# Kernel optimization log

Measured on AMD Instinct MI355X. Metric: run time of the kernel, lower is better.

The kernel has to match this reference:

```python
import jax, jax.numpy as jnp
import numpy as np

B, H, S, D = 2, 16, 2048, 64
NUM_BUCKETS = 32
MAX_DISTANCE = 256


def setup_inputs() -> dict:
    key = jax.random.key(0)
    kq, kk, kv, kb, kl = jax.random.split(key, 5)
    q = jax.random.normal(kq, (B, H, S, D), dtype=jnp.float32)
    k = jax.random.normal(kk, (B, H, S, D), dtype=jnp.float32)
    v = jax.random.normal(kv, (B, H, S, D), dtype=jnp.float32)
    bias_table = jax.random.normal(kb, (NUM_BUCKETS, H), dtype=jnp.float32)
    event_length = jax.random.randint(kl, (B,), 1, S + 1, dtype=jnp.int64)
    return {"q": q, "k": k, "v": v, "bias_table": bias_table, "event_length": event_length}


def _relative_position_bucket(relative_position):
    # T5-style bucketing exactly as the torch module: n = -rel_pos
    half = NUM_BUCKETS // 2  # 16
    n = -relative_position
    is_small = n < half
    # guard log for the branch not taken (n<=0); where() masks it out
    nf = jnp.maximum(n, 1).astype(jnp.float32)
    val_if_large = half + jnp.minimum(
        jnp.log(nf / half) / np.log(MAX_DISTANCE / half) * (NUM_BUCKETS - half),
        NUM_BUCKETS - 1 - half,
    ).astype(jnp.int32)
    ret = jnp.where(is_small, n, val_if_large)
    return jnp.clip(ret, 0, NUM_BUCKETS - 1)


def _compute_bias(bias_table, seq_len):
    ctx = jnp.arange(seq_len)[:, None]
    mem = jnp.arange(seq_len)[None, :]
    rp_bucket = _relative_position_bucket(mem - ctx)  # (S,S)
    values = bias_table[rp_bucket]                    # (S,S,H)
    return jnp.transpose(values, (2, 0, 1))[None]     # (1,H,S,S)


def reference(q, k, v, bias_table, event_length):
    seq_len = q.shape[2]
    head_dim = q.shape[3]
    # scaled QK^T: (B,H,S,S)
    logits = jnp.einsum("bhsd,bhtd->bhst", q, k) / np.sqrt(head_dim).astype(np.float32)
    logits = logits + _compute_bias(bias_table, seq_len)
    # key-side padding mask from per-event lengths
    mask = jnp.arange(seq_len)[None, None, None, :] < event_length[:, None, None, None]
    logits = jnp.where(mask, logits, jnp.float32(-1e9))
    attn = jax.nn.softmax(logits, axis=-1)
    # dropout p=0.01 omitted (eval-mode deterministic reference)
    return jnp.einsum("bhst,bhtd->bhsd", attn, v)
```

## Files before the change

kernel.cpp:

```cpp
#include <hip/hip_runtime.h>

#define B_ 2
#define H_ 16
#define S_ 2048
#define D_ 64
#define BQ 128
#define BK 64
#define NQB (S_ / BQ)
#define LDSTR 72
#define LOG2E 1.4426950408889634f
#define FIXM 10.0f

#if __has_builtin(__builtin_amdgcn_exp2f)
#define EXP2F(x) __builtin_amdgcn_exp2f(x)
#else
#define EXP2F(x) __expf((x) * 0.6931471805599453f)
#endif

typedef _Float16 half8 __attribute__((ext_vector_type(8)));
typedef _Float16 half4 __attribute__((ext_vector_type(4)));
typedef __fp16   fp16x2 __attribute__((ext_vector_type(2)));
typedef float floatx4 __attribute__((ext_vector_type(4)));

typedef _Float16 KlArr[BK][LDSTR];
typedef _Float16 VtArr[D_][LDSTR];
typedef _Float16 PlArr[32][LDSTR];

#define VT_OFF  18432
#define PL_OFF  36864
#define LUT_OFF 55296
#define OX_STR  66
#define LX_OFF  33792

__global__ __launch_bounds__(512, 4)
void t5_attn_kernel(const float* __restrict__ qg_, const float* __restrict__ kg_,
                    const float* __restrict__ vg_, const float* __restrict__ bt,
                    const int* __restrict__ elen, float* __restrict__ outg_)
{
    __shared__ __align__(16) unsigned char smem[56320];
    KlArr* Kl  = reinterpret_cast<KlArr*>(smem);
    VtArr* Vt  = reinterpret_cast<VtArr*>(smem + VT_OFF);
    PlArr* Pl  = reinterpret_cast<PlArr*>(smem + PL_OFF);
    float* lut = reinterpret_cast<float*>(smem + LUT_OFF);

    const int tid  = threadIdx.x;
    const int wave = tid >> 6;
    const int lane = tid & 63;
    const int quad = lane >> 4;
    const int t16  = lane & 15;
    const int wq   = wave >> 1;
    const int kh   = wave & 1;

    const int f    = blockIdx.x + NQB * (blockIdx.y + H_ * blockIdx.z);
    const int qblk = (f >> 3) & 15;
    const int bh   = (f & 7) | ((f >> 7) << 3);
    const int h    = bh & 15;
    const int b    = bh >> 4;

    if (tid < 256) {
        int n = tid;
        int bucket;
        if (n < 16) {
            bucket = n;
        } else {
            int vl = (int)(__log2f((float)n * 0.0625f) * 4.0f);
            bucket = 16 + (vl < 15 ? vl : 15);
        }
        lut[n] = bt[bucket * H_ + h] * LOG2E - FIXM;
    }
    const float sh_next = FIXM - bt[h] * LOG2E;
    const float sh_far  = FIXM - bt[31 * H_ + h] * LOG2E;

    const int len = (elen[1] == 0) ? elen[2 * b] : elen[b];
    const int ntiles = (len + BK - 1) >> 6;

    const size_t bhoff = ((size_t)b * H_ + h) * (size_t)(S_ * D_);
    const float* qptr = qg_ + bhoff;
    const float* kptr = kg_ + bhoff;
    const float* vptr = vg_ + bhoff;
    float*       optr = outg_ + bhoff;

    half8 qf[2][2];
    {
        const float qscale = 0.125f * LOG2E;
        #pragma unroll
        for (int rg = 0; rg < 2; ++rg) {
            const int row = qblk * BQ + wq * 32 + rg * 16 + t16;
            const float* qp = qptr + (size_t)row * D_ + quad * 8;
            #pragma unroll
            for (int c = 0; c < 2; ++c) {
                const float4* p = reinterpret_cast<const float4*>(qp + c * 32);
                float4 x0 = p[0], x1 = p[1];
                half8 hv;
                hv[0] = (_Float16)(x0.x * qscale); hv[1] = (_Float16)(x0.y * qscale);
                hv[2] = (_Float16)(x0.z * qscale); hv[3] = (_Float16)(x0.w * qscale);
                hv[4] = (_Float16)(x1.x * qscale); hv[5] = (_Float16)(x1.y * qscale);
                hv[6] = (_Float16)(x1.z * qscale); hv[7] = (_Float16)(x1.w * qscale);
                qf[rg][c] = hv;
            }
        }
    }

    floatx4 zero4 = {0.f, 0.f, 0.f, 0.f};
    floatx4 acc[2][4];
    float l_[2];
    #pragma unroll
    for (int rg = 0; rg < 2; ++rg) {
        #pragma unroll
        for (int nb = 0; nb < 4; ++nb) acc[rg][nb] = zero4;
        l_[rg] = 0.f;
    }

    const int i_lo = qblk * BQ + wq * 32;

    float4 kx[2];
    float  vx[8];
    auto prefetch = [&](int kt) {
        const int row = tid >> 3;
        const int c8  = (tid & 7) << 3;
        const float4* p = reinterpret_cast<const float4*>(
            kptr + ((size_t)(kt * BK + row) * D_ + c8));
        kx[0] = p[0];
        kx[1] = p[1];
        const int key8 = kt * BK + wave * 8;
        #pragma unroll
        for (int jj = 0; jj < 8; ++jj)
            vx[jj] = vptr[(size_t)(key8 + jj) * D_ + lane];
    };
    auto stage = [&](int buf) {
        const int row = tid >> 3;
        const int c8  = (tid & 7) << 3;
        half8 hv;
        hv[0]=(_Float16)kx[0].x; hv[1]=(_Float16)kx[0].y; hv[2]=(_Float16)kx[0].z; hv[3]=(_Float16)kx[0].w;
        hv[4]=(_Float16)kx[1].x; hv[5]=(_Float16)kx[1].y; hv[6]=(_Float16)kx[1].z; hv[7]=(_Float16)kx[1].w;
        *reinterpret_cast<half8*>(&Kl[buf][row][c8]) = hv;
        half8 vv;
        #pragma unroll
        for (int jj = 0; jj < 8; ++jj) vv[jj] = (_Float16)vx[jj];
        *reinterpret_cast<half8*>(&Vt[buf][lane][wave * 8]) = vv;
    };

    prefetch(0);
    stage(0);
    __syncthreads();

    for (int kt = 0; kt < ntiles; ++kt) {
        const int cur = kt & 1;
        const bool more = (kt + 1) < ntiles;
        if (more) prefetch(kt + 1);

        const int keybase = kt * BK + kh * 32;

        floatx4 sa[2][2];
        #pragma unroll
        for (int rg = 0; rg < 2; ++rg)
            #pragma unroll
            for (int nb = 0; nb < 2; ++nb) sa[rg][nb] = zero4;
        #pragma unroll
        for (int kc = 0; kc < 2; ++kc) {
            #pragma unroll
            for (int nb = 0; nb < 2; ++nb) {
                half8 af = *reinterpret_cast<const half8*>(
                    &Kl[cur][kh * 32 + nb * 16 + t16][kc * 32 + quad * 8]);
                sa[0][nb] = __builtin_amdgcn_mfma_f32_16x16x32_f16(af, qf[0][kc], sa[0][nb], 0, 0, 0);
                sa[1][nb] = __builtin_amdgcn_mfma_f32_16x16x32_f16(af, qf[1][kc], sa[1][nb], 0, 0, 0);
            }
        }

        if (i_lo + 31 <= keybase) {
            #pragma unroll
            for (int rg = 0; rg < 2; ++rg)
                #pragma unroll
                for (int nb = 0; nb < 2; ++nb)
                    #pragma unroll
                    for (int r = 0; r < 4; ++r) sa[rg][nb][r] -= sh_next;
        } else if (i_lo >= keybase + 247) {
            #pragma unroll
            for (int rg = 0; rg < 2; ++rg)
                #pragma unroll
                for (int nb = 0; nb < 2; ++nb)
                    #pragma unroll
                    for (int r = 0; r < 4; ++r) sa[rg][nb][r] -= sh_far;
        } else {
            #pragma unroll
            for (int rg = 0; rg < 2; ++rg) {
                const int d0 = i_lo + rg * 16 + t16 - keybase - quad * 4;
                #pragma unroll
                for (int nb = 0; nb < 2; ++nb) {
                    #pragma unroll
                    for (int r = 0; r < 4; ++r) {
                        int d = d0 - nb * 16 - r;
                        d = d < 0 ? 0 : (d > 255 ? 255 : d);
                        sa[rg][nb][r] += lut[d];
                    }
                }
            }
        }
        if ((kt == ntiles - 1) && (len & 63)) {
            #pragma unroll
            for (int nb = 0; nb < 2; ++nb) {
                #pragma unroll
                for (int r = 0; r < 4; ++r) {
                    bool valid = (keybase + nb * 16 + quad * 4 + r) < len;
                    #pragma unroll
                    for (int rg = 0; rg < 2; ++rg)
                        sa[rg][nb][r] = valid ? sa[rg][nb][r] : -1e30f;
                }
            }
        }

        #pragma unroll
        for (int rg = 0; rg < 2; ++rg) {
            float s = 0.f;
            #pragma unroll
            for (int nb = 0; nb < 2; ++nb)
                #pragma unroll
                for (int r = 0; r < 4; ++r) {
                    sa[rg][nb][r] = EXP2F(sa[rg][nb][r]);
                    s += sa[rg][nb][r];
                }
            l_[rg] += s;
        }

        #pragma unroll
        for (int rg = 0; rg < 2; ++rg) {
            #pragma unroll
            for (int nb = 0; nb < 2; ++nb) {
                fp16x2 lo = __builtin_amdgcn_cvt_pkrtz(sa[rg][nb][0], sa[rg][nb][1]);
                fp16x2 hi = __builtin_amdgcn_cvt_pkrtz(sa[rg][nb][2], sa[rg][nb][3]);
                half4 w;
                w[0] = (_Float16)lo[0]; w[1] = (_Float16)lo[1];
                w[2] = (_Float16)hi[0]; w[3] = (_Float16)hi[1];
                *reinterpret_cast<half4*>(
                    &Pl[wq][rg * 16 + t16][kh * 32 + nb * 16 + quad * 4]) = w;
            }
        }
        asm volatile("s_waitcnt lgkmcnt(0)" ::: "memory");

        {
            half8 a0 = *reinterpret_cast<const half8*>(
                &Pl[wq][t16][kh * 32 + quad * 8]);
            half8 a1 = *reinterpret_cast<const half8*>(
                &Pl[wq][16 + t16][kh * 32 + quad * 8]);
            #pragma unroll
            for (int nb = 0; nb < 4; ++nb) {
                half8 bv = *reinterpret_cast<const half8*>(
                    &Vt[cur][nb * 16 + t16][kh * 32 + quad * 8]);
                acc[0][nb] = __builtin_amdgcn_mfma_f32_16x16x32_f16(a0, bv, acc[0][nb], 0, 0, 0);
                acc[1][nb] = __builtin_amdgcn_mfma_f32_16x16x32_f16(a1, bv, acc[1][nb], 0, 0, 0);
            }
        }

        if (more) stage(cur ^ 1);
        __syncthreads();
    }

    float lh[2];
    #pragma unroll
    for (int rg = 0; rg < 2; ++rg) {
        float lv = l_[rg];
        lv += __shfl_xor(lv, 16, 64);
        lv += __shfl_xor(lv, 32, 64);
        lh[rg] = lv;
    }
    float* Ox = reinterpret_cast<float*>(smem);
    float* Lx = reinterpret_cast<float*>(smem + LX_OFF);
    if (kh == 1) {
        #pragma unroll
        for (int rg = 0; rg < 2; ++rg) {
            #pragma unroll
            for (int nb = 0; nb < 4; ++nb)
                #pragma unroll
                for (int r = 0; r < 4; ++r)
                    Ox[(wq * 32 + rg * 16 + quad * 4 + r) * OX_STR + nb * 16 + t16] =
                        acc[rg][nb][r];
            if (quad == 0) Lx[wq * 32 + rg * 16 + t16] = lh[rg];
        }
    }
    __syncthreads();
    if (kh == 0) {
        #pragma unroll
        for (int rg = 0; rg < 2; ++rg) {
            const float inv = 1.f / (lh[rg] + Lx[wq * 32 + rg * 16 + t16]);
            #pragma unroll
            for (int r = 0; r < 4; ++r) {
                const int rowloc = quad * 4 + r;
                const float invr = __shfl(inv, (lane & 48) | rowloc, 64);
                const int row = qblk * BQ + wq * 32 + rg * 16 + rowloc;
                #pragma unroll
                for (int nb = 0; nb < 4; ++nb)
                    optr[(size_t)row * D_ + nb * 16 + t16] =
                        (acc[rg][nb][r] +
                         Ox[(wq * 32 + rg * 16 + rowloc) * OX_STR + nb * 16 + t16]) * invr;
            }
        }
    }
}

extern "C" void kernel_launch(void* const* d_in, const int* in_sizes, int n_in,
                              void* d_out, int out_size, void* d_ws, size_t ws_size,
                              hipStream_t stream) {
    const float* q  = (const float*)d_in[0];
    const float* k  = (const float*)d_in[1];
    const float* v  = (const float*)d_in[2];
    const float* bt = (const float*)d_in[3];
    const int*   el = (const int*)d_in[4];
    float* out = (float*)d_out;
    dim3 grid(NQB, H_, B_);
    t5_attn_kernel<<<grid, 512, 0, stream>>>(q, k, v, bt, el, out);
}
```

Baseline: 121.9 us.

## Halve query block to 64 rows per block and remap 1-D grid

Shrinks each block's query tile from 128 to 64 rows, so each wave handles one 16-row group instead of two. This doubles the number of blocks, lowers register and LDS use, and raises the occupancy hint to 6 blocks per CU. The grid becomes 1-D with a new bit mapping that keeps blocks sharing the same batch/head close together for L2 reuse. The cost is that every K/V tile is loaded and converted to fp16 twice as often per query row, and the MFMA work per synchronisation halves.

```diff
diff --git a/kernel.cpp b/kernel.cpp
--- a/kernel.cpp
+++ b/kernel.cpp
@@ -4,7 +4,7 @@
 #define H_ 16
 #define S_ 2048
 #define D_ 64
-#define BQ 128
+#define BQ 64
 #define BK 64
 #define NQB (S_ / BQ)
 #define LDSTR 72
@@ -24,20 +24,20 @@
 
 typedef _Float16 KlArr[BK][LDSTR];
 typedef _Float16 VtArr[D_][LDSTR];
-typedef _Float16 PlArr[32][LDSTR];
+typedef _Float16 PlArr[16][LDSTR];
 
 #define VT_OFF  18432
 #define PL_OFF  36864
-#define LUT_OFF 55296
+#define LUT_OFF 46080
 #define OX_STR  66
-#define LX_OFF  33792
-
-__global__ __launch_bounds__(512, 4)
+#define LX_OFF  16896
+
+__global__ __launch_bounds__(512, 6)
 void t5_attn_kernel(const float* __restrict__ qg_, const float* __restrict__ kg_,
                     const float* __restrict__ vg_, const float* __restrict__ bt,
                     const int* __restrict__ elen, float* __restrict__ outg_)
 {
-    __shared__ __align__(16) unsigned char smem[56320];
+    __shared__ __align__(16) unsigned char smem[47104];
     KlArr* Kl  = reinterpret_cast<KlArr*>(smem);
     VtArr* Vt  = reinterpret_cast<VtArr*>(smem + VT_OFF);
     PlArr* Pl  = reinterpret_cast<PlArr*>(smem + PL_OFF);
@@ -51,11 +51,10 @@
     const int wq   = wave >> 1;
     const int kh   = wave & 1;
 
-    const int f    = blockIdx.x + NQB * (blockIdx.y + H_ * blockIdx.z);
-    const int qblk = (f >> 3) & 15;
-    const int bh   = (f & 7) | ((f >> 7) << 3);
-    const int h    = bh & 15;
-    const int b    = bh >> 4;
+    const int f    = blockIdx.x;
+    const int b    = (f >> 3) & 1;
+    const int qblk = (f >> 4) & 31;
+    const int h    = (f & 7) | (((f >> 9) & 1) << 3);
 
     if (tid < 256) {
         int n = tid;
@@ -80,38 +79,31 @@
     const float* vptr = vg_ + bhoff;
     float*       optr = outg_ + bhoff;
 
-    half8 qf[2][2];
+    half8 qf[2];
     {
         const float qscale = 0.125f * LOG2E;
-        #pragma unroll
-        for (int rg = 0; rg < 2; ++rg) {
-            const int row = qblk * BQ + wq * 32 + rg * 16 + t16;
-            const float* qp = qptr + (size_t)row * D_ + quad * 8;
-            #pragma unroll
-            for (int c = 0; c < 2; ++c) {
-                const float4* p = reinterpret_cast<const float4*>(qp + c * 32);
-                float4 x0 = p[0], x1 = p[1];
-                half8 hv;
-                hv[0] = (_Float16)(x0.x * qscale); hv[1] = (_Float16)(x0.y * qscale);
-                hv[2] = (_Float16)(x0.z * qscale); hv[3] = (_Float16)(x0.w * qscale);
-                hv[4] = (_Float16)(x1.x * qscale); hv[5] = (_Float16)(x1.y * qscale);
-                hv[6] = (_Float16)(x1.z * qscale); hv[7] = (_Float16)(x1.w * qscale);
-                qf[rg][c] = hv;
-            }
+        const int row = qblk * BQ + wq * 16 + t16;
+        const float* qp = qptr + (size_t)row * D_ + quad * 8;
+        #pragma unroll
+        for (int c = 0; c < 2; ++c) {
+            const float4* p = reinterpret_cast<const float4*>(qp + c * 32);
+            float4 x0 = p[0], x1 = p[1];
+            half8 hv;
+            hv[0] = (_Float16)(x0.x * qscale); hv[1] = (_Float16)(x0.y * qscale);
+            hv[2] = (_Float16)(x0.z * qscale); hv[3] = (_Float16)(x0.w * qscale);
+            hv[4] = (_Float16)(x1.x * qscale); hv[5] = (_Float16)(x1.y * qscale);
+            hv[6] = (_Float16)(x1.z * qscale); hv[7] = (_Float16)(x1.w * qscale);
+            qf[c] = hv;
         }
     }
 
     floatx4 zero4 = {0.f, 0.f, 0.f, 0.f};
-    floatx4 acc[2][4];
-    float l_[2];
+    floatx4 acc[4];
+    float l_ = 0.f;
     #pragma unroll
-    for (int rg = 0; rg < 2; ++rg) {
-        #pragma unroll
-        for (int nb = 0; nb < 4; ++nb) acc[rg][nb] = zero4;
-        l_[rg] = 0.f;
-    }
-
-    const int i_lo = qblk * BQ + wq * 32;
+    for (int nb = 0; nb < 4; ++nb) acc[nb] = zero4;
+
+    const int i_lo = qblk * BQ + wq * 16;
 
     float4 kx[2];
     float  vx[8];
@@ -151,48 +143,37 @@
 
         const int keybase = kt * BK + kh * 32;
 
-        floatx4 sa[2][2];
-        #pragma unroll
-        for (int rg = 0; rg < 2; ++rg)
-            #pragma unroll
-            for (int nb = 0; nb < 2; ++nb) sa[rg][nb] = zero4;
+        floatx4 sa[2];
+        sa[0] = zero4; sa[1] = zero4;
         #pragma unroll
         for (int kc = 0; kc < 2; ++kc) {
             #pragma unroll
             for (int nb = 0; nb < 2; ++nb) {
                 half8 af = *reinterpret_cast<const half8*>(
                     &Kl[cur][kh * 32 + nb * 16 + t16][kc * 32 + quad * 8]);
-                sa[0][nb] = __builtin_amdgcn_mfma_f32_16x16x32_f16(af, qf[0][kc], sa[0][nb], 0, 0, 0);
-                sa[1][nb] = __builtin_amdgcn_mfma_f32_16x16x32_f16(af, qf[1][kc], sa[1][nb], 0, 0, 0);
-            }
-        }
-
-        if (i_lo + 31 <= keybase) {
-            #pragma unroll
-            for (int rg = 0; rg < 2; ++rg)
-                #pragma unroll
-                for (int nb = 0; nb < 2; ++nb)
-                    #pragma unroll
-                    for (int r = 0; r < 4; ++r) sa[rg][nb][r] -= sh_next;
+                sa[nb] = __builtin_amdgcn_mfma_f32_16x16x32_f16(af, qf[kc], sa[nb], 0, 0, 0);
+            }
+        }
+
+        if (i_lo + 15 <= keybase) {
+            #pragma unroll
+            for (int nb = 0; nb < 2; ++nb)
+                #pragma unroll
+                for (int r = 0; r < 4; ++r) sa[nb][r] -= sh_next;
         } else if (i_lo >= keybase + 247) {
             #pragma unroll
-            for (int rg = 0; rg < 2; ++rg)
-                #pragma unroll
-                for (int nb = 0; nb < 2; ++nb)
-                    #pragma unroll
-                    for (int r = 0; r < 4; ++r) sa[rg][nb][r] -= sh_far;
+            for (int nb = 0; nb < 2; ++nb)
+                #pragma unroll
+                for (int r = 0; r < 4; ++r) sa[nb][r] -= sh_far;
         } else {
-            #pragma unroll
-            for (int rg = 0; rg < 2; ++rg) {
-                const int d0 = i_lo + rg * 16 + t16 - keybase - quad * 4;
-                #pragma unroll
-                for (int nb = 0; nb < 2; ++nb) {
-                    #pragma unroll
-                    for (int r = 0; r < 4; ++r) {
-                        int d = d0 - nb * 16 - r;
-                        d = d < 0 ? 0 : (d > 255 ? 255 : d);
-                        sa[rg][nb][r] += lut[d];
-                    }
+            const int d0 = i_lo + t16 - keybase - quad * 4;
+            #pragma unroll
+            for (int nb = 0; nb < 2; ++nb) {
+                #pragma unroll
+                for (int r = 0; r < 4; ++r) {
+                    int d = d0 - nb * 16 - r;
+                    d = d < 0 ? 0 : (d > 255 ? 255 : d);
+                    sa[nb][r] += lut[d];
                 }
             }
         }
@@ -202,52 +183,43 @@
                 #pragma unroll
                 for (int r = 0; r < 4; ++r) {
                     bool valid = (keybase + nb * 16 + quad * 4 + r) < len;
-                    #pragma unroll
-                    for (int rg = 0; rg < 2; ++rg)
-                        sa[rg][nb][r] = valid ? sa[rg][nb][r] : -1e30f;
+                    sa[nb][r] = valid ? sa[nb][r] : -1e30f;
                 }
             }
         }
 
-        #pragma unroll
-        for (int rg = 0; rg < 2; ++rg) {
+        {
             float s = 0.f;
             #pragma unroll
             for (int nb = 0; nb < 2; ++nb)
                 #pragma unroll
                 for (int r = 0; r < 4; ++r) {
-                    sa[rg][nb][r] = EXP2F(sa[rg][nb][r]);
-                    s += sa[rg][nb][r];
+                    sa[nb][r] = EXP2F(sa[nb][r]);
+                    s += sa[nb][r];
                 }
-            l_[rg] += s;
-        }
-
-        #pragma unroll
-        for (int rg = 0; rg < 2; ++rg) {
-            #pragma unroll
-            for (int nb = 0; nb < 2; ++nb) {
-                fp16x2 lo = __builtin_amdgcn_cvt_pkrtz(sa[rg][nb][0], sa[rg][nb][1]);
-                fp16x2 hi = __builtin_amdgcn_cvt_pkrtz(sa[rg][nb][2], sa[rg][nb][3]);
-                half4 w;
-                w[0] = (_Float16)lo[0]; w[1] = (_Float16)lo[1];
-                w[2] = (_Float16)hi[0]; w[3] = (_Float16)hi[1];
-                *reinterpret_cast<half4*>(
-                    &Pl[wq][rg * 16 + t16][kh * 32 + nb * 16 + quad * 4]) = w;
-            }
+            l_ += s;
+        }
+
+        #pragma unroll
+        for (int nb = 0; nb < 2; ++nb) {
+            fp16x2 lo = __builtin_amdgcn_cvt_pkrtz(sa[nb][0], sa[nb][1]);
+            fp16x2 hi = __builtin_amdgcn_cvt_pkrtz(sa[nb][2], sa[nb][3]);
+            half4 w;
+            w[0] = (_Float16)lo[0]; w[1] = (_Float16)lo[1];
+            w[2] = (_Float16)hi[0]; w[3] = (_Float16)hi[1];
+            *reinterpret_cast<half4*>(
+                &Pl[wq][t16][kh * 32 + nb * 16 + quad * 4]) = w;
         }
         asm volatile("s_waitcnt lgkmcnt(0)" ::: "memory");
 
         {
             half8 a0 = *reinterpret_cast<const half8*>(
                 &Pl[wq][t16][kh * 32 + quad * 8]);
-            half8 a1 = *reinterpret_cast<const half8*>(
-                &Pl[wq][16 + t16][kh * 32 + quad * 8]);
             #pragma unroll
             for (int nb = 0; nb < 4; ++nb) {
                 half8 bv = *reinterpret_cast<const half8*>(
                     &Vt[cur][nb * 16 + t16][kh * 32 + quad * 8]);
-                acc[0][nb] = __builtin_amdgcn_mfma_f32_16x16x32_f16(a0, bv, acc[0][nb], 0, 0, 0);
-                acc[1][nb] = __builtin_amdgcn_mfma_f32_16x16x32_f16(a1, bv, acc[1][nb], 0, 0, 0);
+                acc[nb] = __builtin_amdgcn_mfma_f32_16x16x32_f16(a0, bv, acc[nb], 0, 0, 0);
             }
         }
 
@@ -255,44 +227,33 @@
         __syncthreads();
     }
 
-    float lh[2];
-    #pragma unroll
-    for (int rg = 0; rg < 2; ++rg) {
-        float lv = l_[rg];
-        lv += __shfl_xor(lv, 16, 64);
-        lv += __shfl_xor(lv, 32, 64);
-        lh[rg] = lv;
-    }
+    float lh = l_;
+    lh += __shfl_xor(lh, 16, 64);
+    lh += __shfl_xor(lh, 32, 64);
+
     float* Ox = reinterpret_cast<float*>(smem);
     float* Lx = reinterpret_cast<float*>(smem + LX_OFF);
     if (kh == 1) {
         #pragma unroll
-        for (int rg = 0; rg < 2; ++rg) {
-            #pragma unroll
-            for (int nb = 0; nb < 4; ++nb)
-                #pragma unroll
-                for (int r = 0; r < 4; ++r)
-                    Ox[(wq * 32 + rg * 16 + quad * 4 + r) * OX_STR + nb * 16 + t16] =
-                        acc[rg][nb][r];
-            if (quad == 0) Lx[wq * 32 + rg * 16 + t16] = lh[rg];
-        }
+        for (int nb = 0; nb < 4; ++nb)
+            #pragma unroll
+            for (int r = 0; r < 4; ++r)
+                Ox[(wq * 16 + quad * 4 + r) * OX_STR + nb * 16 + t16] = acc[nb][r];
+        if (quad == 0) Lx[wq * 16 + t16] = lh;
     }
     __syncthreads();
     if (kh == 0) {
-        #pragma unroll
-        for (int rg = 0; rg < 2; ++rg) {
-            const float inv = 1.f / (lh[rg] + Lx[wq * 32 + rg * 16 + t16]);
-            #pragma unroll
-            for (int r = 0; r < 4; ++r) {
-                const int rowloc = quad * 4 + r;
-                const float invr = __shfl(inv, (lane & 48) | rowloc, 64);
-                const int row = qblk * BQ + wq * 32 + rg * 16 + rowloc;
-                #pragma unroll
-                for (int nb = 0; nb < 4; ++nb)
-                    optr[(size_t)row * D_ + nb * 16 + t16] =
-                        (acc[rg][nb][r] +
-                         Ox[(wq * 32 + rg * 16 + rowloc) * OX_STR + nb * 16 + t16]) * invr;
-            }
+        const float inv = 1.f / (lh + Lx[wq * 16 + t16]);
+        #pragma unroll
+        for (int r = 0; r < 4; ++r) {
+            const int rowloc = quad * 4 + r;
+            const float invr = __shfl(inv, (lane & 48) | rowloc, 64);
+            const int row = qblk * BQ + wq * 16 + rowloc;
+            #pragma unroll
+            for (int nb = 0; nb < 4; ++nb)
+                optr[(size_t)row * D_ + nb * 16 + t16] =
+                    (acc[nb][r] +
+                     Ox[(wq * 16 + rowloc) * OX_STR + nb * 16 + t16]) * invr;
         }
     }
 }
@@ -306,6 +267,6 @@
     const float* bt = (const float*)d_in[3];
     const int*   el = (const int*)d_in[4];
     float* out = (float*)d_out;
-    dim3 grid(NQB, H_, B_);
+    dim3 grid(NQB * H_ * B_);
     t5_attn_kernel<<<grid, 512, 0, stream>>>(q, k, v, bt, el, out);
 }
```

Result: slower. 148.5 us (+21.9%).

## Balance key-tile work across batches with split-K blocks and workspace merge

Applied to the files above, without the earlier changes.

Adds a split kernel that counts the total valid key tiles across both batches and divides that tile range evenly between two blocks per (head, query block), so every block does about the same work no matter how the event lengths differ. When a block's range straddles the batch boundary, each half writes its partial numerator and row sums to a workspace slot, and an atomic counter picks whichever block finishes second to merge them and normalise. The change also adds s_setprio around the MFMA sections. The cost is an extra memset launch, workspace traffic and atomics; the path is used only when a large enough workspace is supplied.

```diff
diff --git a/kernel.cpp b/kernel.cpp
--- a/kernel.cpp
+++ b/kernel.cpp
@@ -32,6 +32,352 @@
 #define OX_STR  66
 #define LX_OFF  33792
 
+#define SLOT_F  8320
+#define WS_NEED (1024u + 512u * SLOT_F * 4u)
+
+__global__ __launch_bounds__(512, 4)
+void t5_attn_split(const float* __restrict__ qg_, const float* __restrict__ kg_,
+                   const float* __restrict__ vg_, const float* __restrict__ bt,
+                   const int* __restrict__ elen, float* __restrict__ outg_,
+                   float* __restrict__ ws)
+{
+    __shared__ __align__(16) unsigned char smem[56320];
+    __shared__ int s_old;
+    KlArr* Kl  = reinterpret_cast<KlArr*>(smem);
+    VtArr* Vt  = reinterpret_cast<VtArr*>(smem + VT_OFF);
+    PlArr* Pl  = reinterpret_cast<PlArr*>(smem + PL_OFF);
+    float* lut = reinterpret_cast<float*>(smem + LUT_OFF);
+
+    const int tid  = threadIdx.x;
+    const int wave = tid >> 6;
+    const int lane = tid & 63;
+    const int quad = lane >> 4;
+    const int t16  = lane & 15;
+    const int wq   = wave >> 1;
+    const int kh   = wave & 1;
+
+    const int f = blockIdx.x;
+    const int w = f >> 8;
+    const int p = f & 255;
+    const int h    = p & 15;
+    const int qblk = p >> 4;
+
+    if (tid < 256) {
+        int n = tid;
+        int bucket;
+        if (n < 16) {
+            bucket = n;
+        } else {
+            int vl = (int)(__log2f((float)n * 0.0625f) * 4.0f);
+            bucket = 16 + (vl < 15 ? vl : 15);
+        }
+        lut[n] = bt[bucket * H_ + h] * LOG2E - FIXM;
+    }
+    const float sh_next = FIXM - bt[h] * LOG2E;
+    const float sh_far  = FIXM - bt[31 * H_ + h] * LOG2E;
+
+    const int l0 = elen[0];
+    const int l1 = (elen[1] == 0) ? elen[2] : elen[1];
+    const int nt0 = (l0 + 63) >> 6;
+    const int nt1 = (l1 + 63) >> 6;
+    const int T    = nt0 + nt1;
+    const int half = (T + 1) >> 1;
+    const int sA = w ? half : 0;
+    const int eA = w ? T    : half;
+    const int shared_b = (half < nt0) ? 0 : ((half > nt0) ? 1 : -1);
+
+    unsigned* flags = reinterpret_cast<unsigned*>(ws);
+    float* part = ws + 256;
+
+    const int i_lo = qblk * BQ + wq * 32;
+
+    for (int bseg = 0; bseg < 2; ++bseg) {
+        const int lo = bseg ? nt0 : 0;
+        const int hi = bseg ? T   : nt0;
+        int s = sA > lo ? sA : lo;
+        int e = eA < hi ? eA : hi;
+        if (s >= e) continue;
+        const int ktA = s - lo, ktB = e - lo;
+        const int len = bseg ? l1 : l0;
+        const int ntb = bseg ? nt1 : nt0;
+        const bool is_partial = (bseg == shared_b);
+
+        const size_t bhoff = ((size_t)bseg * H_ + h) * (size_t)(S_ * D_);
+        const float* qptr = qg_ + bhoff;
+        const float* kptr = kg_ + bhoff;
+        const float* vptr = vg_ + bhoff;
+        float*       optr = outg_ + bhoff;
+
+        half8 qf[2][2];
+        {
+            const float qscale = 0.125f * LOG2E;
+            #pragma unroll
+            for (int rg = 0; rg < 2; ++rg) {
+                const int row = qblk * BQ + wq * 32 + rg * 16 + t16;
+                const float* qp = qptr + (size_t)row * D_ + quad * 8;
+                #pragma unroll
+                for (int c = 0; c < 2; ++c) {
+                    const float4* pq = reinterpret_cast<const float4*>(qp + c * 32);
+                    float4 x0 = pq[0], x1 = pq[1];
+                    half8 hv;
+                    hv[0] = (_Float16)(x0.x * qscale); hv[1] = (_Float16)(x0.y * qscale);
+                    hv[2] = (_Float16)(x0.z * qscale); hv[3] = (_Float16)(x0.w * qscale);
+                    hv[4] = (_Float16)(x1.x * qscale); hv[5] = (_Float16)(x1.y * qscale);
+                    hv[6] = (_Float16)(x1.z * qscale); hv[7] = (_Float16)(x1.w * qscale);
+                    qf[rg][c] = hv;
+                }
+            }
+        }
+
+        floatx4 zero4 = {0.f, 0.f, 0.f, 0.f};
+        floatx4 acc[2][4];
+        float l_[2];
+        #pragma unroll
+        for (int rg = 0; rg < 2; ++rg) {
+            #pragma unroll
+            for (int nb = 0; nb < 4; ++nb) acc[rg][nb] = zero4;
+            l_[rg] = 0.f;
+        }
+
+        float4 kx[2];
+        float  vx[8];
+        auto prefetch = [&](int kt) {
+            const int row = tid >> 3;
+            const int c8  = (tid & 7) << 3;
+            const float4* pp = reinterpret_cast<const float4*>(
+                kptr + ((size_t)(kt * BK + row) * D_ + c8));
+            kx[0] = pp[0];
+            kx[1] = pp[1];
+            const int key8 = kt * BK + wave * 8;
+            #pragma unroll
+            for (int jj = 0; jj < 8; ++jj)
+                vx[jj] = vptr[(size_t)(key8 + jj) * D_ + lane];
+        };
+        auto stage = [&](int buf) {
+            const int row = tid >> 3;
+            const int c8  = (tid & 7) << 3;
+            half8 hv;
+            hv[0]=(_Float16)kx[0].x; hv[1]=(_Float16)kx[0].y; hv[2]=(_Float16)kx[0].z; hv[3]=(_Float16)kx[0].w;
+            hv[4]=(_Float16)kx[1].x; hv[5]=(_Float16)kx[1].y; hv[6]=(_Float16)kx[1].z; hv[7]=(_Float16)kx[1].w;
+            *reinterpret_cast<half8*>(&Kl[buf][row][c8]) = hv;
+            half8 vv;
+            #pragma unroll
+            for (int jj = 0; jj < 8; ++jj) vv[jj] = (_Float16)vx[jj];
+            *reinterpret_cast<half8*>(&Vt[buf][lane][wave * 8]) = vv;
+        };
+
+        prefetch(ktA);
+        stage(ktA & 1);
+        __syncthreads();
+
+        for (int kt = ktA; kt < ktB; ++kt) {
+            const int cur = kt & 1;
+            const bool more = (kt + 1) < ktB;
+            if (more) prefetch(kt + 1);
+
+            const int keybase = kt * BK + kh * 32;
+
+            floatx4 sa[2][2];
+            #pragma unroll
+            for (int rg = 0; rg < 2; ++rg)
+                #pragma unroll
+                for (int nb = 0; nb < 2; ++nb) sa[rg][nb] = zero4;
+            __builtin_amdgcn_s_setprio(1);
+            #pragma unroll
+            for (int kc = 0; kc < 2; ++kc) {
+                #pragma unroll
+                for (int nb = 0; nb < 2; ++nb) {
+                    half8 af = *reinterpret_cast<const half8*>(
+                        &Kl[cur][kh * 32 + nb * 16 + t16][kc * 32 + quad * 8]);
+                    sa[0][nb] = __builtin_amdgcn_mfma_f32_16x16x32_f16(af, qf[0][kc], sa[0][nb], 0, 0, 0);
+                    sa[1][nb] = __builtin_amdgcn_mfma_f32_16x16x32_f16(af, qf[1][kc], sa[1][nb], 0, 0, 0);
+                }
+            }
+            __builtin_amdgcn_s_setprio(0);
+
+            if (i_lo + 31 <= keybase) {
+                #pragma unroll
+                for (int rg = 0; rg < 2; ++rg)
+                    #pragma unroll
+                    for (int nb = 0; nb < 2; ++nb)
+                        #pragma unroll
+                        for (int r = 0; r < 4; ++r) sa[rg][nb][r] -= sh_next;
+            } else if (i_lo >= keybase + 247) {
+                #pragma unroll
+                for (int rg = 0; rg < 2; ++rg)
+                    #pragma unroll
+                    for (int nb = 0; nb < 2; ++nb)
+                        #pragma unroll
+                        for (int r = 0; r < 4; ++r) sa[rg][nb][r] -= sh_far;
+            } else {
+                #pragma unroll
+                for (int rg = 0; rg < 2; ++rg) {
+                    const int d0 = i_lo + rg * 16 + t16 - keybase - quad * 4;
+                    #pragma unroll
+                    for (int nb = 0; nb < 2; ++nb) {
+                        #pragma unroll
+                        for (int r = 0; r < 4; ++r) {
+                            int d = d0 - nb * 16 - r;
+                            d = d < 0 ? 0 : (d > 255 ? 255 : d);
+                            sa[rg][nb][r] += lut[d];
+                        }
+                    }
+                }
+            }
+            if ((kt == ntb - 1) && (len & 63)) {
+                #pragma unroll
+                for (int nb = 0; nb < 2; ++nb) {
+                    #pragma unroll
+                    for (int r = 0; r < 4; ++r) {
+                        bool valid = (keybase + nb * 16 + quad * 4 + r) < len;
+                        #pragma unroll
+                        for (int rg = 0; rg < 2; ++rg)
+                            sa[rg][nb][r] = valid ? sa[rg][nb][r] : -1e30f;
+                    }
+                }
+            }
+
+            #pragma unroll
+            for (int rg = 0; rg < 2; ++rg) {
+                float ssum = 0.f;
+                #pragma unroll
+                for (int nb = 0; nb < 2; ++nb)
+                    #pragma unroll
+                    for (int r = 0; r < 4; ++r) {
+                        sa[rg][nb][r] = EXP2F(sa[rg][nb][r]);
+                        ssum += sa[rg][nb][r];
+                    }
+                l_[rg] += ssum;
+            }
+
+            #pragma unroll
+            for (int rg = 0; rg < 2; ++rg) {
+                #pragma unroll
+                for (int nb = 0; nb < 2; ++nb) {
+                    fp16x2 plo = __builtin_amdgcn_cvt_pkrtz(sa[rg][nb][0], sa[rg][nb][1]);
+                    fp16x2 phi = __builtin_amdgcn_cvt_pkrtz(sa[rg][nb][2], sa[rg][nb][3]);
+                    half4 wv;
+                    wv[0] = (_Float16)plo[0]; wv[1] = (_Float16)plo[1];
+                    wv[2] = (_Float16)phi[0]; wv[3] = (_Float16)phi[1];
+                    *reinterpret_cast<half4*>(
+                        &Pl[wq][rg * 16 + t16][kh * 32 + nb * 16 + quad * 4]) = wv;
+                }
+            }
+            asm volatile("s_waitcnt lgkmcnt(0)" ::: "memory");
+
+            {
+                half8 a0 = *reinterpret_cast<const half8*>(
+                    &Pl[wq][t16][kh * 32 + quad * 8]);
+                half8 a1 = *reinterpret_cast<const half8*>(
+                    &Pl[wq][16 + t16][kh * 32 + quad * 8]);
+                __builtin_amdgcn_s_setprio(1);
+                #pragma unroll
+                for (int nb = 0; nb < 4; ++nb) {
+                    half8 bv = *reinterpret_cast<const half8*>(
+                        &Vt[cur][nb * 16 + t16][kh * 32 + quad * 8]);
+                    acc[0][nb] = __builtin_amdgcn_mfma_f32_16x16x32_f16(a0, bv, acc[0][nb], 0, 0, 0);
+                    acc[1][nb] = __builtin_amdgcn_mfma_f32_16x16x32_f16(a1, bv, acc[1][nb], 0, 0, 0);
+                }
+                __builtin_amdgcn_s_setprio(0);
+            }
+
+            if (more) stage(cur ^ 1);
+            __syncthreads();
+        }
+
+        float lh[2];
+        #pragma unroll
+        for (int rg = 0; rg < 2; ++rg) {
+            float lv = l_[rg];
+            lv += __shfl_xor(lv, 16, 64);
+            lv += __shfl_xor(lv, 32, 64);
+            lh[rg] = lv;
+        }
+        float* Ox = reinterpret_cast<float*>(smem);
+        float* Lx = reinterpret_cast<float*>(smem + LX_OFF);
+        if (kh == 1) {
+            #pragma unroll
+            for (int rg = 0; rg < 2; ++rg) {
+                #pragma unroll
+                for (int nb = 0; nb < 4; ++nb)
+                    #pragma unroll
+                    for (int r = 0; r < 4; ++r)
+                        Ox[(wq * 32 + rg * 16 + quad * 4 + r) * OX_STR + nb * 16 + t16] =
+                            acc[rg][nb][r];
+                if (quad == 0) Lx[wq * 32 + rg * 16 + t16] = lh[rg];
+            }
+        }
+        __syncthreads();
+
+        if (!is_partial) {
+            if (kh == 0) {
+                #pragma unroll
+                for (int rg = 0; rg < 2; ++rg) {
+                    const float inv = 1.f / (lh[rg] + Lx[wq * 32 + rg * 16 + t16]);
+                    #pragma unroll
+                    for (int r = 0; r < 4; ++r) {
+                        const int rowloc = quad * 4 + r;
+                        const float invr = __shfl(inv, (lane & 48) | rowloc, 64);
+                        const int row = qblk * BQ + wq * 32 + rg * 16 + rowloc;
+                        #pragma unroll
+                        for (int nb = 0; nb < 4; ++nb)
+                            optr[(size_t)row * D_ + nb * 16 + t16] =
+                                (acc[rg][nb][r] +
+                                 Ox[(wq * 32 + rg * 16 + rowloc) * OX_STR + nb * 16 + t16]) * inv
+                                * 0.f + (acc[rg][nb][r] +
+                                 Ox[(wq * 32 + rg * 16 + rowloc) * OX_STR + nb * 16 + t16]) * invr;
+                    }
+                }
+            }
+        } else {
+            float* slot = part + (size_t)(p * 2 + w) * SLOT_F;
+            if (kh == 0) {
+                #pragma unroll
+                for (int rg = 0; rg < 2; ++rg) {
+                    #pragma unroll
+                    for (int r = 0; r < 4; ++r) {
+                        const int rowloc = quad * 4 + r;
+                        const int rloc = wq * 32 + rg * 16 + rowloc;
+                        #pragma unroll
+                        for (int nb = 0; nb < 4; ++nb)
+                            slot[rloc * D_ + nb * 16 + t16] =
+                                acc[rg][nb][r] +
+                                Ox[rloc * OX_STR + nb * 16 + t16];
+                    }
+                    if (quad == 0)
+                        slot[8192 + wq * 32 + rg * 16 + t16] =
+                            lh[rg] + Lx[wq * 32 + rg * 16 + t16];
+                }
+            }
+            __syncthreads();
+            if (tid == 0) {
+                __threadfence();
+                s_old = (int)atomicAdd(&flags[p], 1u);
+            }
+            __syncthreads();
+            if (s_old == 1) {
+                __threadfence();
+                const float* s0 = part + (size_t)(p * 2 + 0) * SLOT_F;
+                const float* s1 = part + (size_t)(p * 2 + 1) * SLOT_F;
+                const int row = tid >> 2;
+                const int c16 = (tid & 3) << 4;
+                const float inv = 1.f / (s0[8192 + row] + s1[8192 + row]);
+                float* od = optr + (size_t)(qblk * BQ + row) * D_ + c16;
+                #pragma unroll
+                for (int j = 0; j < 4; ++j) {
+                    float4 a = *reinterpret_cast<const float4*>(s0 + row * D_ + c16 + j * 4);
+                    float4 bvv = *reinterpret_cast<const float4*>(s1 + row * D_ + c16 + j * 4);
+                    float4 o;
+                    o.x = (a.x + bvv.x) * inv; o.y = (a.y + bvv.y) * inv;
+                    o.z = (a.z + bvv.z) * inv; o.w = (a.w + bvv.w) * inv;
+                    *reinterpret_cast<float4*>(od + j * 4) = o;
+                }
+            }
+        }
+        __syncthreads();
+    }
+}
+
 __global__ __launch_bounds__(512, 4)
 void t5_attn_kernel(const float* __restrict__ qg_, const float* __restrict__ kg_,
                     const float* __restrict__ vg_, const float* __restrict__ bt,
@@ -60,9 +406,8 @@
     if (tid < 256) {
         int n = tid;
         int bucket;
-        if (n < 16) {
-            bucket = n;
-        } else {
+        if (n < 16) bucket = n;
+        else {
             int vl = (int)(__log2f((float)n * 0.0625f) * 4.0f);
             bucket = 16 + (vl < 15 ? vl : 15);
         }
@@ -89,8 +434,8 @@
             const float* qp = qptr + (size_t)row * D_ + quad * 8;
             #pragma unroll
             for (int c = 0; c < 2; ++c) {
-                const float4* p = reinterpret_cast<const float4*>(qp + c * 32);
-                float4 x0 = p[0], x1 = p[1];
+                const float4* pq = reinterpret_cast<const float4*>(qp + c * 32);
+                float4 x0 = pq[0], x1 = pq[1];
                 half8 hv;
                 hv[0] = (_Float16)(x0.x * qscale); hv[1] = (_Float16)(x0.y * qscale);
                 hv[2] = (_Float16)(x0.z * qscale); hv[3] = (_Float16)(x0.w * qscale);
@@ -118,10 +463,10 @@
     auto prefetch = [&](int kt) {
         const int row = tid >> 3;
         const int c8  = (tid & 7) << 3;
-        const float4* p = reinterpret_cast<const float4*>(
+        const float4* pp = reinterpret_cast<const float4*>(
             kptr + ((size_t)(kt * BK + row) * D_ + c8));
-        kx[0] = p[0];
-        kx[1] = p[1];
+        kx[0] = pp[0];
+        kx[1] = pp[1];
         const int key8 = kt * BK + wave * 8;
         #pragma unroll
         for (int jj = 0; jj < 8; ++jj)
@@ -211,28 +556,28 @@
 
         #pragma unroll
         for (int rg = 0; rg < 2; ++rg) {
-            float s = 0.f;
+            float ssum = 0.f;
             #pragma unroll
             for (int nb = 0; nb < 2; ++nb)
                 #pragma unroll
                 for (int r = 0; r < 4; ++r) {
                     sa[rg][nb][r] = EXP2F(sa[rg][nb][r]);
-                    s += sa[rg][nb][r];
-                }
-            l_[rg] += s;
+                    ssum += sa[rg][nb][r];
+                }
+            l_[rg] += ssum;
         }
 
         #pragma unroll
         for (int rg = 0; rg < 2; ++rg) {
             #pragma unroll
             for (int nb = 0; nb < 2; ++nb) {
-                fp16x2 lo = __builtin_amdgcn_cvt_pkrtz(sa[rg][nb][0], sa[rg][nb][1]);
-                fp16x2 hi = __builtin_amdgcn_cvt_pkrtz(sa[rg][nb][2], sa[rg][nb][3]);
-                half4 w;
-                w[0] = (_Float16)lo[0]; w[1] = (_Float16)lo[1];
-                w[2] = (_Float16)hi[0]; w[3] = (_Float16)hi[1];
+                fp16x2 plo = __builtin_amdgcn_cvt_pkrtz(sa[rg][nb][0], sa[rg][nb][1]);
+                fp16x2 phi = __builtin_amdgcn_cvt_pkrtz(sa[rg][nb][2], sa[rg][nb][3]);
+                half4 wv;
+                wv[0] = (_Float16)plo[0]; wv[1] = (_Float16)plo[1];
+                wv[2] = (_Float16)phi[0]; wv[3] = (_Float16)phi[1];
                 *reinterpret_cast<half4*>(
-                    &Pl[wq][rg * 16 + t16][kh * 32 + nb * 16 + quad * 4]) = w;
+                    &Pl[wq][rg * 16 + t16][kh * 32 + nb * 16 + quad * 4]) = wv;
             }
         }
         asm volatile("s_waitcnt lgkmcnt(0)" ::: "memory");
@@ -306,6 +651,12 @@
     const float* bt = (const float*)d_in[3];
     const int*   el = (const int*)d_in[4];
     float* out = (float*)d_out;
-    dim3 grid(NQB, H_, B_);
-    t5_attn_kernel<<<grid, 512, 0, stream>>>(q, k, v, bt, el, out);
+    if (d_ws != nullptr && ws_size >= (size_t)WS_NEED) {
+        hipMemsetAsync(d_ws, 0, 1024, stream);
+        t5_attn_split<<<dim3(512), 512, 0, stream>>>(q, k, v, bt, el, out,
+                                                     (float*)d_ws);
+    } else {
+        dim3 grid(NQB, H_, B_);
+        t5_attn_kernel<<<grid, 512, 0, stream>>>(q, k, v, bt, el, out);
+    }
 }
```

Result: slower. 244.6 us (+100.7%).

## Feed P directly from registers into PV MFMA, drop LDS round-trip

Applied to the files above, without the earlier changes.

Instead of writing the softmax probabilities to a per-wave LDS buffer and reading them back, the kernel packs the exp scores in registers and uses them as the A operand of 16x16x16 MFMAs. The QK^T score layout already matches that operand layout. V is read from LDS as two half4 pieces to match. This removes the LDS stores, the lgkmcnt wait and the reloads, and shrinks shared memory from 56KB to 37KB, which may allow more resident blocks. In exchange it issues twice as many smaller MFMAs, and s_setprio hints are added around the MFMA sections.

```diff
diff --git a/kernel.cpp b/kernel.cpp
--- a/kernel.cpp
+++ b/kernel.cpp
@@ -24,11 +24,9 @@
 
 typedef _Float16 KlArr[BK][LDSTR];
 typedef _Float16 VtArr[D_][LDSTR];
-typedef _Float16 PlArr[32][LDSTR];
 
 #define VT_OFF  18432
-#define PL_OFF  36864
-#define LUT_OFF 55296
+#define LUT_OFF 36864
 #define OX_STR  66
 #define LX_OFF  33792
 
@@ -37,10 +35,9 @@
                     const float* __restrict__ vg_, const float* __restrict__ bt,
                     const int* __restrict__ elen, float* __restrict__ outg_)
 {
-    __shared__ __align__(16) unsigned char smem[56320];
+    __shared__ __align__(16) unsigned char smem[37888];
     KlArr* Kl  = reinterpret_cast<KlArr*>(smem);
     VtArr* Vt  = reinterpret_cast<VtArr*>(smem + VT_OFF);
-    PlArr* Pl  = reinterpret_cast<PlArr*>(smem + PL_OFF);
     float* lut = reinterpret_cast<float*>(smem + LUT_OFF);
 
     const int tid  = threadIdx.x;
@@ -89,8 +86,8 @@
             const float* qp = qptr + (size_t)row * D_ + quad * 8;
             #pragma unroll
             for (int c = 0; c < 2; ++c) {
-                const float4* p = reinterpret_cast<const float4*>(qp + c * 32);
-                float4 x0 = p[0], x1 = p[1];
+                const float4* pq = reinterpret_cast<const float4*>(qp + c * 32);
+                float4 x0 = pq[0], x1 = pq[1];
                 half8 hv;
                 hv[0] = (_Float16)(x0.x * qscale); hv[1] = (_Float16)(x0.y * qscale);
                 hv[2] = (_Float16)(x0.z * qscale); hv[3] = (_Float16)(x0.w * qscale);
@@ -113,15 +110,24 @@
 
     const int i_lo = qblk * BQ + wq * 32;
 
+    auto pack4 = [](const floatx4& v) -> half4 {
+        fp16x2 lo = __builtin_amdgcn_cvt_pkrtz(v[0], v[1]);
+        fp16x2 hi = __builtin_amdgcn_cvt_pkrtz(v[2], v[3]);
+        half4 w;
+        w[0] = (_Float16)lo[0]; w[1] = (_Float16)lo[1];
+        w[2] = (_Float16)hi[0]; w[3] = (_Float16)hi[1];
+        return w;
+    };
+
     float4 kx[2];
     float  vx[8];
     auto prefetch = [&](int kt) {
         const int row = tid >> 3;
         const int c8  = (tid & 7) << 3;
-        const float4* p = reinterpret_cast<const float4*>(
+        const float4* pp = reinterpret_cast<const float4*>(
             kptr + ((size_t)(kt * BK + row) * D_ + c8));
-        kx[0] = p[0];
-        kx[1] = p[1];
+        kx[0] = pp[0];
+        kx[1] = pp[1];
         const int key8 = kt * BK + wave * 8;
         #pragma unroll
         for (int jj = 0; jj < 8; ++jj)
@@ -156,6 +162,7 @@
         for (int rg = 0; rg < 2; ++rg)
             #pragma unroll
             for (int nb = 0; nb < 2; ++nb) sa[rg][nb] = zero4;
+        __builtin_amdgcn_s_setprio(1);
         #pragma unroll
         for (int kc = 0; kc < 2; ++kc) {
             #pragma unroll
@@ -166,6 +173,7 @@
                 sa[1][nb] = __builtin_amdgcn_mfma_f32_16x16x32_f16(af, qf[1][kc], sa[1][nb], 0, 0, 0);
             }
         }
+        __builtin_amdgcn_s_setprio(0);
 
         if (i_lo + 31 <= keybase) {
             #pragma unroll
@@ -211,44 +219,35 @@
 
         #pragma unroll
         for (int rg = 0; rg < 2; ++rg) {
-            float s = 0.f;
+            float ssum = 0.f;
             #pragma unroll
             for (int nb = 0; nb < 2; ++nb)
                 #pragma unroll
                 for (int r = 0; r < 4; ++r) {
                     sa[rg][nb][r] = EXP2F(sa[rg][nb][r]);
-                    s += sa[rg][nb][r];
+                    ssum += sa[rg][nb][r];
                 }
-            l_[rg] += s;
-        }
-
-        #pragma unroll
-        for (int rg = 0; rg < 2; ++rg) {
-            #pragma unroll
-            for (int nb = 0; nb < 2; ++nb) {
-                fp16x2 lo = __builtin_amdgcn_cvt_pkrtz(sa[rg][nb][0], sa[rg][nb][1]);
-                fp16x2 hi = __builtin_amdgcn_cvt_pkrtz(sa[rg][nb][2], sa[rg][nb][3]);
-                half4 w;
-                w[0] = (_Float16)lo[0]; w[1] = (_Float16)lo[1];
-                w[2] = (_Float16)hi[0]; w[3] = (_Float16)hi[1];
-                *reinterpret_cast<half4*>(
-                    &Pl[wq][rg * 16 + t16][kh * 32 + nb * 16 + quad * 4]) = w;
-            }
-        }
-        asm volatile("s_waitcnt lgkmcnt(0)" ::: "memory");
+            l_[rg] += ssum;
+        }
 
         {
-            half8 a0 = *reinterpret_cast<const half8*>(
-                &Pl[wq][t16][kh * 32 + quad * 8]);
-            half8 a1 = *reinterpret_cast<const half8*>(
-                &Pl[wq][16 + t16][kh * 32 + quad * 8]);
+            half4 aA0 = pack4(sa[0][0]);
+            half4 aB0 = pack4(sa[0][1]);
+            half4 aA1 = pack4(sa[1][0]);
+            half4 aB1 = pack4(sa[1][1]);
+            __builtin_amdgcn_s_setprio(1);
             #pragma unroll
             for (int nb = 0; nb < 4; ++nb) {
-                half8 bv = *reinterpret_cast<const half8*>(
-                    &Vt[cur][nb * 16 + t16][kh * 32 + quad * 8]);
-                acc[0][nb] = __builtin_amdgcn_mfma_f32_16x16x32_f16(a0, bv, acc[0][nb], 0, 0, 0);
-                acc[1][nb] = __builtin_amdgcn_mfma_f32_16x16x32_f16(a1, bv, acc[1][nb], 0, 0, 0);
-            }
+                half4 bv0 = *reinterpret_cast<const half4*>(
+                    &Vt[cur][nb * 16 + t16][kh * 32 + quad * 4]);
+                half4 bv1 = *reinterpret_cast<const half4*>(
+                    &Vt[cur][nb * 16 + t16][kh * 32 + 16 + quad * 4]);
+                acc[0][nb] = __builtin_amdgcn_mfma_f32_16x16x16f16(aA0, bv0, acc[0][nb], 0, 0, 0);
+                acc[0][nb] = __builtin_amdgcn_mfma_f32_16x16x16f16(aB0, bv1, acc[0][nb], 0, 0, 0);
+                acc[1][nb] = __builtin_amdgcn_mfma_f32_16x16x16f16(aA1, bv0, acc[1][nb], 0, 0, 0);
+                acc[1][nb] = __builtin_amdgcn_mfma_f32_16x16x16f16(aB1, bv1, acc[1][nb], 0, 0, 0);
+            }
+            __builtin_amdgcn_s_setprio(0);
         }
 
         if (more) stage(cur ^ 1);
```

New measurement: 122.0 us. No clear change (+0.2%).
